# Kernel tuning notes

Hardware: AMD Instinct MI355X
Metric: run time of the kernel (lower is better)

The kernel has to match this reference:

```python
import jax, jax.numpy as jnp
import numpy as np

WS = (8, 8, 8)          # window_size (d, h, w) -- all equal
N_TOK = WS[0] * WS[1] * WS[2]   # 512
DIM = 192
HEADS = 6
HEAD_DIM = DIM // HEADS  # 32
B_ = 64                  # num_windows * batch (batch = 1)


def _build_rel_coords_table():
    # matches torch: meshgrid of arange(-(w-1), w) per axis, normalized, *8, signed log2
    r = np.arange(-(WS[0] - 1), WS[0], dtype=np.float32)
    tab = np.stack(np.meshgrid(r, r, r, indexing='ij'), axis=-1)[None]  # (1,15,15,15,3)
    tab = tab / (WS[0] - 1)
    tab = tab * 8.0
    tab = np.sign(tab) * np.log2(np.abs(tab) + 1.0) / np.log2(8.0)
    return tab.astype(np.float32)


def _build_rel_pos_index():
    c = np.arange(WS[0])
    coords = np.stack(np.meshgrid(c, c, c, indexing='ij'))          # (3, 8, 8, 8)
    flat = coords.reshape(3, -1)                                     # (3, N)
    rel = flat[:, :, None] - flat[:, None, :]                        # (3, N, N)
    rel = rel.transpose(1, 2, 0).copy()                              # (N, N, 3)
    rel += WS[0] - 1
    rel[:, :, 0] *= (2 * WS[1] - 1) * (2 * WS[2] - 1)
    rel[:, :, 1] *= 2 * WS[2] - 1
    return rel.sum(-1).astype(np.int32)                              # (N, N)


def setup_inputs() -> dict:
    key = jax.random.key(0)
    ks = jax.random.split(key, 8)
    x = jax.random.normal(ks[0], (B_, N_TOK, DIM), dtype=jnp.float32)
    # 0 / -inf style additive mask (use large negative finite for stability)
    m = jax.random.uniform(ks[1], (B_, N_TOK, N_TOK))
    mask = jnp.where(m < 0.1, jnp.float32(-1e4), jnp.float32(0.0))
    w_qkv = jax.random.normal(ks[2], (3 * DIM, DIM), dtype=jnp.float32) * (DIM ** -0.5)
    q_bias = jnp.zeros((DIM,), jnp.float32)
    v_bias = jnp.zeros((DIM,), jnp.float32)
    cpb_w1 = jax.random.normal(ks[3], (512, 3), dtype=jnp.float32) * 0.3
    cpb_b1 = jnp.zeros((512,), jnp.float32)
    cpb_w2 = jax.random.normal(ks[4], (HEADS, 512), dtype=jnp.float32) * 0.05
    rel_coords_table = jnp.asarray(_build_rel_coords_table())
    rel_pos_index = jnp.asarray(_build_rel_pos_index())
    return {"x": x, "mask": mask, "w_qkv": w_qkv, "q_bias": q_bias,
            "v_bias": v_bias, "cpb_w1": cpb_w1, "cpb_b1": cpb_b1,
            "cpb_w2": cpb_w2, "rel_coords_table": rel_coords_table,
            "rel_pos_index": rel_pos_index}


def reference(x, mask, w_qkv, q_bias, v_bias, cpb_w1, cpb_b1, cpb_w2,
              rel_coords_table, rel_pos_index):
    Bw, N, C = x.shape
    H, D = HEADS, HEAD_DIM
    # qkv projection with bias = cat(q_bias, zeros, v_bias)
    qkv_bias = jnp.concatenate([q_bias, jnp.zeros_like(v_bias), v_bias])
    qkv = x @ w_qkv.T + qkv_bias                       # (Bw, N, 3C)
    qkv = qkv.reshape(Bw, N, 3, H, D).transpose(2, 0, 3, 1, 4)
    q, k, v = qkv[0], qkv[1], qkv[2]                   # (Bw, H, N, D)
    # continuous position bias MLP: 3 -> 512 -> H
    tab = rel_coords_table.reshape(-1, 3)              # (3375, 3)
    tab = jax.nn.relu(tab @ cpb_w1.T + cpb_b1) @ cpb_w2.T  # (3375, H)
    bias = tab[rel_pos_index.reshape(-1)].reshape(N, N, H)
    bias = 16.0 * jax.nn.sigmoid(bias.transpose(2, 0, 1))  # (H, N, N)
    # SDPA with additive mask (standard 1/sqrt(D) scaling, as in forward_flash)
    scale = jnp.float32(1.0 / np.sqrt(D))
    scores = jnp.einsum('bhnd,bhmd->bhnm', q, k) * scale
    scores = scores + mask[:, None, :, :] + bias[None]
    attn = jax.nn.softmax(scores, axis=-1)
    out = jnp.einsum('bhnm,bhmd->bhnd', attn, v)       # (Bw, H, N, D)
    return out
```

## Files before the change

kernel.cpp:

```cpp
#include <hip/hip_runtime.h>
#include <hip/hip_bf16.h>


typedef __bf16 bf16x8 __attribute__((ext_vector_type(8)));
typedef __bf16 bf16x4v __attribute__((ext_vector_type(4)));
typedef float  f32x4  __attribute__((ext_vector_type(4)));
typedef _Float16 f16x4 __attribute__((ext_vector_type(4)));
typedef _Float16 f16x8 __attribute__((ext_vector_type(8)));
typedef unsigned uint2v __attribute__((ext_vector_type(2)));
typedef unsigned long long u64;

#define LOG2E 1.4426950408889634f

__device__ __forceinline__ bf16x8 cvt2_bf16x8(f32x4 a, f32x4 b) {
  bf16x8 r;
  r[0] = (__bf16)a[0]; r[1] = (__bf16)a[1]; r[2] = (__bf16)a[2]; r[3] = (__bf16)a[3];
  r[4] = (__bf16)b[0]; r[5] = (__bf16)b[1]; r[6] = (__bf16)b[2]; r[7] = (__bf16)b[3];
  return r;
}

__device__ __forceinline__ unsigned pack2bf(float a, float b) {
  unsigned short ua = __builtin_bit_cast(unsigned short, (__bf16)a);
  unsigned short ub = __builtin_bit_cast(unsigned short, (__bf16)b);
  return (unsigned)ua | ((unsigned)ub << 16);
}

__device__ __forceinline__ bf16x8 frag_from_words(unsigned w0, unsigned w1,
                                                  unsigned w2, unsigned w3) {
  union { unsigned u[4]; bf16x8 v; } f;
  f.u[0] = w0; f.u[1] = w1; f.u[2] = w2; f.u[3] = w3;
  return f.v;
}

#define PREP_WCONV 108
#define PREP_CPB   3375
#define PREP_GRID  (PREP_WCONV + PREP_CPB)

__global__ __launch_bounds__(256) void prep_kernel(
    const float* __restrict__ w, __bf16* __restrict__ wbf,
    const float* __restrict__ table, const float* __restrict__ w1,
    const float* __restrict__ b1, const float* __restrict__ w2,
    float* __restrict__ tab6)
{
  __shared__ float red[4][6];
  int blk = blockIdx.x;
  if (blk < PREP_WCONV) {
    int t = blk * 256 + threadIdx.x;
    f32x4 v = *(const f32x4*)(w + (size_t)t * 4);
    bf16x4v o;
    o[0] = (__bf16)v[0]; o[1] = (__bf16)v[1]; o[2] = (__bf16)v[2]; o[3] = (__bf16)v[3];
    *(bf16x4v*)(wbf + (size_t)t * 4) = o;
  } else {
    int p = blk - PREP_WCONV;
    float c0 = table[p * 3 + 0], c1 = table[p * 3 + 1], c2 = table[p * 3 + 2];
    float acc[6] = {0.f, 0.f, 0.f, 0.f, 0.f, 0.f};
#pragma unroll
    for (int jj = 0; jj < 2; ++jj) {
      int j = threadIdx.x + jj * 256;
      float hv = w1[j * 3 + 0] * c0 + w1[j * 3 + 1] * c1 + w1[j * 3 + 2] * c2 + b1[j];
      hv = fmaxf(hv, 0.0f);
#pragma unroll
      for (int t = 0; t < 6; ++t) acc[t] += w2[t * 512 + j] * hv;
    }
#pragma unroll
    for (int t = 0; t < 6; ++t) {
      acc[t] += __shfl_xor(acc[t], 1);
      acc[t] += __shfl_xor(acc[t], 2);
      acc[t] += __shfl_xor(acc[t], 4);
      acc[t] += __shfl_xor(acc[t], 8);
      acc[t] += __shfl_xor(acc[t], 16);
      acc[t] += __shfl_xor(acc[t], 32);
    }
    int wave = threadIdx.x >> 6;
    if ((threadIdx.x & 63) == 0)
#pragma unroll
      for (int t = 0; t < 6; ++t) red[wave][t] = acc[t];
    __syncthreads();
    if (threadIdx.x < 6) {
      int t = threadIdx.x;
      float s = red[0][t] + red[1][t] + red[2][t] + red[3][t];
      float sig = 16.0f / (1.0f + expf(-s));
      tab6[p * 6 + t] = sig * LOG2E;
    }
  }
}

#define MID_QKV  1024
#define MID_MB   4096
#define MID_BIAS 1366
#define MID_GRID (MID_QKV + MID_MB + MID_BIAS)

__global__ __launch_bounds__(192) void mid_kernel(
    const float* __restrict__ x,
    const __bf16* __restrict__ wbf,
    const float* __restrict__ qb,
    const float* __restrict__ vb,
    __bf16* __restrict__ Qo,
    __bf16* __restrict__ Ko,
    __bf16* __restrict__ Vt,
    const int* __restrict__ relidx,
    const float* __restrict__ tab6,
    _Float16* __restrict__ biasH,
    const float* __restrict__ m,
    u64* __restrict__ bits)
{
  __shared__ __bf16 tile[2][32][72];
  if (blockIdx.x >= MID_QKV + MID_MB) {
    for (int ij = (blockIdx.x - MID_QKV - MID_MB) * 192 + threadIdx.x;
         ij < 262144; ij += MID_BIAS * 192) {
      int i = ij >> 9, p = ij & 511;
      int jblk = p >> 6, g = (p >> 4) & 3, kf = (p >> 2) & 3, t = p & 3;
      int j = (jblk << 6) + kf * 16 + g * 4 + t;
      int idx = relidx[(i << 9) + j];
#pragma unroll
      for (int t6 = 0; t6 < 6; ++t6)
        biasH[(size_t)t6 * 262144 + ij] = (_Float16)tab6[idx * 6 + t6];
    }
    return;
  }
  if (blockIdx.x >= MID_QKV) {
    int li16 = threadIdx.x & 15;
    for (size_t t = (size_t)(blockIdx.x - MID_QKV) * 192 + threadIdx.x;
         t < 4194304ull; t += (size_t)MID_MB * 192) {
      f32x4 v = *(const f32x4*)(m + t * 4);
      unsigned nib = (v[0] == 0.f ? 1u : 0u) | (v[1] == 0.f ? 2u : 0u) |
                     (v[2] == 0.f ? 4u : 0u) | (v[3] == 0.f ? 8u : 0u);
      u64 part = (u64)nib << (4 * li16);
      part |= __shfl_xor(part, 1);
      part |= __shfl_xor(part, 2);
      part |= __shfl_xor(part, 4);
      part |= __shfl_xor(part, 8);
      if (li16 == 0) {
        int w_ = (int)(t >> 4);
        int b = w_ >> 12, i = (w_ >> 3) & 511, jw = w_ & 7;
        bits[(((size_t)b * 8 + jw) << 9) + i] = part;
      }
    }
    return;
  }
  const float CQ = 0.17677669529663687f * LOG2E;
  int lane = threadIdx.x & 63, wave = threadIdx.x >> 6;
  int g = lane >> 4, li = lane & 15;
  int rowbase = blockIdx.x * 32;
  int b = rowbase >> 9, nbase = rowbase & 511;

  bf16x8 a[2][6];
#pragma unroll
  for (int mm = 0; mm < 2; ++mm)
#pragma unroll
    for (int k = 0; k < 6; ++k) {
      const float* xp = x + (size_t)(rowbase + mm * 16 + li) * 192 + k * 32 + 8 * g;
      f32x4 x0 = *(const f32x4*)xp;
      f32x4 x1 = *(const f32x4*)(xp + 4);
      a[mm][k] = cvt2_bf16x8(x0, x1);
    }

  for (int ncl = 0; ncl < 3; ++ncl) {
    int nc = wave * 3 + ncl;
    f32x4 acc[2][4];
#pragma unroll
    for (int n = 0; n < 4; ++n) {
      int r = nc * 64 + n * 16 + li;
      float bb = 0.0f;
      if (r < 192) bb = qb[r];
      else if (r >= 384) bb = vb[r - 384];
      f32x4 v = {bb, bb, bb, bb};
      acc[0][n] = v; acc[1][n] = v;
    }
#pragma unroll
    for (int k = 0; k < 6; ++k) {
#pragma unroll
      for (int n = 0; n < 4; ++n) {
        bf16x8 bf = *(const bf16x8*)(wbf + (size_t)(nc * 64 + n * 16 + li) * 192 + k * 32 + 8 * g);
        acc[0][n] = __builtin_amdgcn_mfma_f32_16x16x32_bf16(a[0][k], bf, acc[0][n], 0, 0, 0);
        acc[1][n] = __builtin_amdgcn_mfma_f32_16x16x32_bf16(a[1][k], bf, acc[1][n], 0, 0, 0);
      }
    }
    if (wave < 2) {
      float scale = (wave == 0) ? CQ : 1.0f;
#pragma unroll
      for (int n = 0; n < 4; ++n)
#pragma unroll
        for (int mm = 0; mm < 2; ++mm)
#pragma unroll
          for (int t = 0; t < 4; ++t)
            tile[wave][mm * 16 + 4 * g + t][n * 16 + li] = (__bf16)(acc[mm][n][t] * scale);
      int tok = lane & 31, hh = lane >> 5;
      int h = (nc * 2 + hh) % 6;
      __bf16* base = (wave == 0) ? Qo : Ko;
      __bf16* dst = base + ((size_t)(b * 6 + h) * 512 + nbase + tok) * 32;
#pragma unroll
      for (int kq = 0; kq < 4; ++kq)
        *(bf16x8*)(dst + kq * 8) = *(const bf16x8*)&tile[wave][tok][hh * 32 + kq * 8];
    } else {
#pragma unroll
      for (int n = 0; n < 4; ++n) {
        int rr = nc * 64 + n * 16 + li - 384, h = rr >> 5, d = rr & 31;
#pragma unroll
        for (int mm = 0; mm < 2; ++mm) {
          int nn = nbase + mm * 16 + 4 * g;
          bf16x4v pk;
#pragma unroll
          for (int t = 0; t < 4; ++t) pk[t] = (__bf16)acc[mm][n][t];
          *(bf16x4v*)(Vt + ((size_t)(b * 6 + h) * 32 + d) * 512 + nn) = pk;
        }
      }
    }
  }
}

__global__ __launch_bounds__(256, 3) void attn_kernel(
    const u64* __restrict__ bits,
    const _Float16* __restrict__ biasH,
    const __bf16* __restrict__ Qw,
    const __bf16* __restrict__ Kw,
    const __bf16* __restrict__ Vt,
    float* __restrict__ out)
{
  int hw = blockIdx.x;
  int wgid = (hw & 7) * 96 + (hw >> 3);
  int qt = wgid & 1, h = (wgid >> 1) % 6, b = wgid / 12;
  int lane = threadIdx.x & 63, wave = threadIdx.x >> 6;
  int g = lane >> 4, li = lane & 15;
  int qbase = qt * 256 + wave * 64;
  int bh = b * 6 + h;
  int gsh = 4 * g;

  const __bf16* Qb = Qw + (size_t)bh * 16384;
  const __bf16* Kb = Kw + (size_t)bh * 16384;
  const __bf16* Vb = Vt + (size_t)bh * 16384;
  const _Float16* biasb = biasH + (size_t)h * 262144 + g * 16;
  const u64* bitsb = bits + (size_t)b * 4096;

  bf16x8 qfrag[4];
#pragma unroll
  for (int qf = 0; qf < 4; ++qf)
    qfrag[qf] = *(const bf16x8*)(Qb + (qbase + qf * 16 + li) * 32 + 8 * g);

  f32x4 oacc[4][2] = {};
  float l_part[4] = {0.f, 0.f, 0.f, 0.f};

  for (int kb = 0; kb < 8; ++kb) {
    int j64 = kb * 64;
    u64 mb[4];
#pragma unroll
    for (int qf = 0; qf < 4; ++qf)
      mb[qf] = bitsb[(kb << 9) + qbase + qf * 16 + li] >> gsh;
    bf16x8 kfr[4];
#pragma unroll
    for (int kf = 0; kf < 4; ++kf)
      kfr[kf] = *(const bf16x8*)(Kb + (j64 + kf * 16 + li) * 32 + 8 * g);
    bf16x8 vfr[2][2];
#pragma unroll
    for (int df = 0; df < 2; ++df)
#pragma unroll
      for (int c = 0; c < 2; ++c)
        vfr[df][c] = *(const bf16x8*)(Vb + (df * 16 + li) * 512 + j64 + c * 32 + 8 * g);
    f16x8 hv8[4][2];
#pragma unroll
    for (int qf = 0; qf < 4; ++qf) {
      const _Float16* bp = biasb + (size_t)(qbase + qf * 16 + li) * 512 + j64;
      hv8[qf][0] = *(const f16x8*)(bp);
      hv8[qf][1] = *(const f16x8*)(bp + 8);
    }

#pragma unroll
    for (int c = 0; c < 2; ++c) {
      unsigned lo[4][2], hi[4][2];
#pragma unroll
      for (int kfl = 0; kfl < 2; ++kfl) {
        int kf = c * 2 + kfl;
        const int hsel = kf >> 1, hoff = (kf & 1) * 4;
#pragma unroll
        for (int qf = 0; qf < 4; ++qf) {
          f16x8 hb = hv8[qf][hsel];
          f32x4 ci = {(float)hb[hoff], (float)hb[hoff + 1],
                      (float)hb[hoff + 2], (float)hb[hoff + 3]};
          f32x4 s = __builtin_amdgcn_mfma_f32_16x16x32_bf16(kfr[kf], qfrag[qf], ci, 0, 0, 0);
          unsigned nib = (unsigned)(mb[qf] >> (kf * 16)) & 15u;
          float p0 = (nib & 1u) ? __builtin_amdgcn_exp2f(s[0]) : 0.0f;
          float p1 = (nib & 2u) ? __builtin_amdgcn_exp2f(s[1]) : 0.0f;
          float p2 = (nib & 4u) ? __builtin_amdgcn_exp2f(s[2]) : 0.0f;
          float p3 = (nib & 8u) ? __builtin_amdgcn_exp2f(s[3]) : 0.0f;
          l_part[qf] += (p0 + p1) + (p2 + p3);
          lo[qf][kfl] = pack2bf(p0, p1);
          hi[qf][kfl] = pack2bf(p2, p3);
        }
      }
#pragma unroll
      for (int qf = 0; qf < 4; ++qf) {
        uint2v sl = __builtin_amdgcn_permlane32_swap(lo[qf][0], lo[qf][1], 0, 0);
        uint2v wl = __builtin_amdgcn_permlane16_swap(sl.x, sl.y, 0, 0);
        uint2v sh = __builtin_amdgcn_permlane32_swap(hi[qf][0], hi[qf][1], 0, 0);
        uint2v wh = __builtin_amdgcn_permlane16_swap(sh.x, sh.y, 0, 0);
        bf16x8 pf = frag_from_words(wl.x, wh.x, wl.y, wh.y);
#pragma unroll
        for (int df = 0; df < 2; ++df)
          oacc[qf][df] = __builtin_amdgcn_mfma_f32_16x16x32_bf16(vfr[df][c], pf, oacc[qf][df], 0, 0, 0);
      }
    }
  }

#pragma unroll
  for (int qf = 0; qf < 4; ++qf) {
    float l = l_part[qf];
    l += __shfl_xor(l, 16);
    l += __shfl_xor(l, 32);
    float linv = 1.0f / l;
#pragma unroll
    for (int df = 0; df < 2; ++df) {
      float* op = out + ((size_t)bh * 512 + qbase + qf * 16 + li) * 32 + df * 16 + 4 * g;
      f32x4 r = oacc[qf][df] * linv;
      *(f32x4*)op = r;
    }
  }
}

extern "C" void kernel_launch(void* const* d_in, const int* in_sizes, int n_in,
                              void* d_out, int out_size, void* d_ws, size_t ws_size,
                              hipStream_t stream) {
  const float* x    = (const float*)d_in[0];
  const float* mask = (const float*)d_in[1];
  const float* wqkv = (const float*)d_in[2];
  const float* qb   = (const float*)d_in[3];
  const float* vb   = (const float*)d_in[4];
  const float* w1   = (const float*)d_in[5];
  const float* b1   = (const float*)d_in[6];
  const float* w2   = (const float*)d_in[7];
  const float* tbl  = (const float*)d_in[8];
  const int*   ridx = (const int*)d_in[9];
  float* out = (float*)d_out;

  char* ws = (char*)d_ws;
  float*    tab6  = (float*)(ws);
  _Float16* biasH = (_Float16*)(ws + 81920);
  u64*      bits  = (u64*)(ws + 81920 + 3145728);
  __bf16*   wbf   = (__bf16*)(ws + 81920 + 3145728 + 2097152);
  __bf16*   Q     = (__bf16*)(ws + 81920 + 3145728 + 2097152 + 262144);
  __bf16*   K     = Q + (size_t)64 * 6 * 512 * 32;
  __bf16*   Vt    = K + (size_t)64 * 6 * 512 * 32;

  prep_kernel<<<PREP_GRID, 256, 0, stream>>>(wqkv, wbf, tbl, w1, b1, w2, tab6);
  mid_kernel<<<MID_GRID, 192, 0, stream>>>(x, wbf, qb, vb, Q, K, Vt,
                                           ridx, tab6, biasH, mask, bits);
  attn_kernel<<<768, 256, 0, stream>>>(bits, biasH, Q, K, Vt, out);
}
```

Baseline: 121.7 us.

## Move mask bit-packing into prep kernel and vectorize bias gather

Mask-to-bitmask conversion moves from the mid kernel into the prep kernel, with each thread now handling 8 floats per iteration instead of 4. The bias table is padded to a stride of 8 so the bias expansion can read it with aligned vector loads. That expansion now processes 4 output elements per thread using int4 index loads and f16x4 stores. The aim is to balance work across the two pre-attention kernels and cut scalar gather and store traffic, at the cost of more work in the prep kernel.

Result: faster. 118.1 us (-2.9%).

```diff
diff --git a/kernel.cpp b/kernel.cpp
--- a/kernel.cpp
+++ b/kernel.cpp
@@ -8,6 +8,7 @@
 typedef _Float16 f16x4 __attribute__((ext_vector_type(4)));
 typedef _Float16 f16x8 __attribute__((ext_vector_type(8)));
 typedef unsigned uint2v __attribute__((ext_vector_type(2)));
+typedef int int4v __attribute__((ext_vector_type(4)));
 typedef unsigned long long u64;
 
 #define LOG2E 1.4426950408889634f
@@ -34,13 +35,16 @@
 
 #define PREP_WCONV 108
 #define PREP_CPB   3375
-#define PREP_GRID  (PREP_WCONV + PREP_CPB)
+#define PREP_WC    (PREP_WCONV + PREP_CPB)
+#define PREP_MB    2048
+#define PREP_GRID  (PREP_WC + PREP_MB)
 
 __global__ __launch_bounds__(256) void prep_kernel(
     const float* __restrict__ w, __bf16* __restrict__ wbf,
     const float* __restrict__ table, const float* __restrict__ w1,
     const float* __restrict__ b1, const float* __restrict__ w2,
-    float* __restrict__ tab6)
+    float* __restrict__ tab6,
+    const float* __restrict__ m, u64* __restrict__ bits)
 {
   __shared__ float red[4][6];
   int blk = blockIdx.x;
@@ -50,7 +54,7 @@
     bf16x4v o;
     o[0] = (__bf16)v[0]; o[1] = (__bf16)v[1]; o[2] = (__bf16)v[2]; o[3] = (__bf16)v[3];
     *(bf16x4v*)(wbf + (size_t)t * 4) = o;
-  } else {
+  } else if (blk < PREP_WC) {
     int p = blk - PREP_WCONV;
     float c0 = table[p * 3 + 0], c1 = table[p * 3 + 1], c2 = table[p * 3 + 2];
     float acc[6] = {0.f, 0.f, 0.f, 0.f, 0.f, 0.f};
@@ -80,15 +84,36 @@
       int t = threadIdx.x;
       float s = red[0][t] + red[1][t] + red[2][t] + red[3][t];
       float sig = 16.0f / (1.0f + expf(-s));
-      tab6[p * 6 + t] = sig * LOG2E;
+      tab6[p * 8 + t] = sig * LOG2E;
+    }
+  } else {
+    int li8 = threadIdx.x & 7;
+    for (size_t t = (size_t)(blk - PREP_WC) * 256 + threadIdx.x;
+         t < 2097152ull; t += (size_t)PREP_MB * 256) {
+      const float* mp = m + t * 8;
+      f32x4 v0 = *(const f32x4*)mp;
+      f32x4 v1 = *(const f32x4*)(mp + 4);
+      unsigned byte =
+          (v0[0] == 0.f ? 1u : 0u)  | (v0[1] == 0.f ? 2u : 0u) |
+          (v0[2] == 0.f ? 4u : 0u)  | (v0[3] == 0.f ? 8u : 0u) |
+          (v1[0] == 0.f ? 16u : 0u) | (v1[1] == 0.f ? 32u : 0u) |
+          (v1[2] == 0.f ? 64u : 0u) | (v1[3] == 0.f ? 128u : 0u);
+      u64 part = (u64)byte << (8 * li8);
+      part |= __shfl_xor(part, 1);
+      part |= __shfl_xor(part, 2);
+      part |= __shfl_xor(part, 4);
+      if (li8 == 0) {
+        int w_ = (int)(t >> 3);
+        int b = w_ >> 12, i = (w_ >> 3) & 511, jw = w_ & 7;
+        bits[(((size_t)b * 8 + jw) << 9) + i] = part;
+      }
     }
   }
 }
 
 #define MID_QKV  1024
-#define MID_MB   4096
-#define MID_BIAS 1366
-#define MID_GRID (MID_QKV + MID_MB + MID_BIAS)
+#define MID_BIAS 342
+#define MID_GRID (MID_QKV + MID_BIAS)
 
 __global__ __launch_bounds__(192) void mid_kernel(
     const float* __restrict__ x,
@@ -100,40 +125,30 @@
     __bf16* __restrict__ Vt,
     const int* __restrict__ relidx,
     const float* __restrict__ tab6,
-    _Float16* __restrict__ biasH,
-    const float* __restrict__ m,
-    u64* __restrict__ bits)
+    _Float16* __restrict__ biasH)
 {
   __shared__ __bf16 tile[2][32][72];
-  if (blockIdx.x >= MID_QKV + MID_MB) {
-    for (int ij = (blockIdx.x - MID_QKV - MID_MB) * 192 + threadIdx.x;
-         ij < 262144; ij += MID_BIAS * 192) {
+  if (blockIdx.x >= MID_QKV) {
+    for (int q4 = (blockIdx.x - MID_QKV) * 192 + threadIdx.x; q4 < 65536;
+         q4 += MID_BIAS * 192) {
+      int ij = q4 * 4;
       int i = ij >> 9, p = ij & 511;
-      int jblk = p >> 6, g = (p >> 4) & 3, kf = (p >> 2) & 3, t = p & 3;
-      int j = (jblk << 6) + kf * 16 + g * 4 + t;
-      int idx = relidx[(i << 9) + j];
-#pragma unroll
-      for (int t6 = 0; t6 < 6; ++t6)
-        biasH[(size_t)t6 * 262144 + ij] = (_Float16)tab6[idx * 6 + t6];
-    }
-    return;
-  }
-  if (blockIdx.x >= MID_QKV) {
-    int li16 = threadIdx.x & 15;
-    for (size_t t = (size_t)(blockIdx.x - MID_QKV) * 192 + threadIdx.x;
-         t < 4194304ull; t += (size_t)MID_MB * 192) {
-      f32x4 v = *(const f32x4*)(m + t * 4);
-      unsigned nib = (v[0] == 0.f ? 1u : 0u) | (v[1] == 0.f ? 2u : 0u) |
-                     (v[2] == 0.f ? 4u : 0u) | (v[3] == 0.f ? 8u : 0u);
-      u64 part = (u64)nib << (4 * li16);
-      part |= __shfl_xor(part, 1);
-      part |= __shfl_xor(part, 2);
-      part |= __shfl_xor(part, 4);
-      part |= __shfl_xor(part, 8);
-      if (li16 == 0) {
-        int w_ = (int)(t >> 4);
-        int b = w_ >> 12, i = (w_ >> 3) & 511, jw = w_ & 7;
-        bits[(((size_t)b * 8 + jw) << 9) + i] = part;
+      int jblk = p >> 6, g = (p >> 4) & 3, kf = (p >> 2) & 3;
+      int j = (jblk << 6) + kf * 16 + g * 4;
+      int4v idx4 = *(const int4v*)(relidx + (i << 9) + j);
+      float val[6][4];
+#pragma unroll
+      for (int u = 0; u < 4; ++u) {
+        f32x4 lo = *(const f32x4*)(tab6 + (size_t)idx4[u] * 8);
+        f32x4 hi = *(const f32x4*)(tab6 + (size_t)idx4[u] * 8 + 4);
+        val[0][u] = lo[0]; val[1][u] = lo[1]; val[2][u] = lo[2];
+        val[3][u] = lo[3]; val[4][u] = hi[0]; val[5][u] = hi[1];
+      }
+#pragma unroll
+      for (int t6 = 0; t6 < 6; ++t6) {
+        f16x4 o = {(_Float16)val[t6][0], (_Float16)val[t6][1],
+                   (_Float16)val[t6][2], (_Float16)val[t6][3]};
+        *(f16x4*)(biasH + (size_t)t6 * 262144 + ij) = o;
       }
     }
     return;
@@ -333,15 +348,16 @@
 
   char* ws = (char*)d_ws;
   float*    tab6  = (float*)(ws);
-  _Float16* biasH = (_Float16*)(ws + 81920);
-  u64*      bits  = (u64*)(ws + 81920 + 3145728);
-  __bf16*   wbf   = (__bf16*)(ws + 81920 + 3145728 + 2097152);
-  __bf16*   Q     = (__bf16*)(ws + 81920 + 3145728 + 2097152 + 262144);
+  _Float16* biasH = (_Float16*)(ws + 131072);
+  u64*      bits  = (u64*)(ws + 131072 + 3145728);
+  __bf16*   wbf   = (__bf16*)(ws + 131072 + 3145728 + 2097152);
+  __bf16*   Q     = (__bf16*)(ws + 131072 + 3145728 + 2097152 + 262144);
   __bf16*   K     = Q + (size_t)64 * 6 * 512 * 32;
   __bf16*   Vt    = K + (size_t)64 * 6 * 512 * 32;
 
-  prep_kernel<<<PREP_GRID, 256, 0, stream>>>(wqkv, wbf, tbl, w1, b1, w2, tab6);
+  prep_kernel<<<PREP_GRID, 256, 0, stream>>>(wqkv, wbf, tbl, w1, b1, w2, tab6,
+                                             mask, bits);
   mid_kernel<<<MID_GRID, 192, 0, stream>>>(x, wbf, qb, vb, Q, K, Vt,
-                                           ridx, tab6, biasH, mask, bits);
+                                           ridx, tab6, biasH);
   attn_kernel<<<768, 256, 0, stream>>>(bits, biasH, Q, K, Vt, out);
 }
```
